# Kernel tuning notes

Measured on AMD Instinct MI355X. Metric: run time of the kernel, lower is better.

The kernel has to match this reference:

```python
import jax, jax.numpy as jnp
import numpy as np

D_MODEL = 512
N_HEADS = 8
HEAD_DIM = D_MODEL // N_HEADS
B, T = 128, 256


def setup_inputs() -> dict:
    key = jax.random.key(0)
    ks = jax.random.split(key, 5)
    s = 1.0 / np.sqrt(D_MODEL)
    return {
        "x": jax.random.normal(ks[0], (B, T, D_MODEL), dtype=jnp.float32),
        "W_qkv": jax.random.uniform(ks[1], (D_MODEL, 3 * D_MODEL), jnp.float32, -s, s),
        "b_qkv": jax.random.uniform(ks[2], (3 * D_MODEL,), jnp.float32, -s, s),
        "W_out": jax.random.uniform(ks[3], (D_MODEL, D_MODEL), jnp.float32, -s, s),
        "b_out": jax.random.uniform(ks[4], (D_MODEL,), jnp.float32, -s, s),
    }


def reference(x, W_qkv, b_qkv, W_out, b_out):
    Bsz, Tlen, C = x.shape
    H, hd = N_HEADS, HEAD_DIM
    qkv = x @ W_qkv + b_qkv                       # [B,T,3C]
    qkv = qkv.reshape(Bsz, Tlen, 3, H, hd).transpose(2, 0, 3, 1, 4)  # [3,B,H,T,hd]
    q, k, v = qkv[0], qkv[1], qkv[2]
    att = jnp.einsum('bhtd,bhsd->bhts', q, k) * (1.0 / np.sqrt(hd))  # [B,H,T,T]
    causal = jnp.tril(jnp.ones((Tlen, Tlen), dtype=bool))
    att = jnp.where(causal, att, -jnp.inf)
    att = jax.nn.softmax(att, axis=-1)
    y = jnp.einsum('bhts,bhsd->bhtd', att, v)     # [B,H,T,hd]
    y = y.transpose(0, 2, 1, 3).reshape(Bsz, Tlen, C)
    return y @ W_out + b_out
```

## Files before the change

kernel.cpp:

```cpp
#include <hip/hip_runtime.h>
#include <hip/hip_bf16.h>

typedef __attribute__((ext_vector_type(4))) float f32x4;
typedef __attribute__((ext_vector_type(8))) short s16x8;
typedef unsigned short u16;

__device__ __forceinline__ u16 f2bf(float f) {
    union { float f; unsigned int u; } a; a.f = f;
    unsigned int u = a.u;
    unsigned int lsb = (u >> 16) & 1u;
    u += 0x7fffu + lsb;
    return (u16)(u >> 16);
}

__device__ __forceinline__ void gll16(const u16* g, u16* l) {
    __builtin_amdgcn_global_load_lds(
        (const __attribute__((address_space(1))) unsigned int*)g,
        (__attribute__((address_space(3))) unsigned int*)l, 16, 0, 0);
}


__global__ __launch_bounds__(256) void cvt_all_kernel(const float* __restrict__ x,
                                                      const float* __restrict__ W_qkv,
                                                      const float* __restrict__ W_out,
                                                      u16* __restrict__ xb,
                                                      u16* __restrict__ WqkvT,
                                                      u16* __restrict__ WoutT) {
    int bid = blockIdx.x;
    if (bid < 16384) {
        int i = bid * 256 + threadIdx.x;
        float4 v = ((const float4*)x)[i];
        ushort4 o;
        o.x = f2bf(v.x); o.y = f2bf(v.y); o.z = f2bf(v.z); o.w = f2bf(v.w);
        ((ushort4*)xb)[i] = o;
    } else if (bid < 16768) {
        int id = (bid - 16384) * 256 + threadIdx.x;
        int n = id % 1536, kg = id / 1536;
        union { u16 h[8]; int4 v; } o;
#pragma unroll
        for (int e = 0; e < 8; ++e) o.h[e] = f2bf(W_qkv[(kg * 8 + e) * 1536 + n]);
        *(int4*)&WqkvT[n * 512 + kg * 8] = o.v;
    } else {
        int id = (bid - 16768) * 256 + threadIdx.x;
        int n = id % 512, kg = id / 512;
        union { u16 h[8]; int4 v; } o;
#pragma unroll
        for (int e = 0; e < 8; ++e) o.h[e] = f2bf(W_out[(kg * 8 + e) * 512 + n]);
        *(int4*)&WoutT[n * 512 + kg * 8] = o.v;
    }
}


template<int K>
__device__ __forceinline__ void stage256(const u16* __restrict__ A, const u16* __restrict__ Bt,
                                         int m0, int n0, int kt, u16* As, u16* Bs) {
    const int lane = threadIdx.x & 63, w = threadIdx.x >> 6;
    const int lr = lane >> 3, lg = lane & 7;
    const int sgA = lg ^ lr;
#pragma unroll
    for (int j = 0; j < 4; ++j) {
        const int blk = w * 4 + j;
        gll16(&A[(m0 + blk * 8 + lr) * K + kt + sgA * 8], &As[blk * 512]);
    }
#pragma unroll
    for (int j = 0; j < 4; ++j) {
        const int blk = w * 4 + j;
        const int sgB = lg ^ ((2 * j + (lr >> 2)) & 7);
        gll16(&Bt[(n0 + blk * 8 + lr) * K + kt + sgB * 8], &Bs[blk * 512]);
    }
}


template<int K>
__device__ __forceinline__ void gemm_tile256(const u16* __restrict__ A, const u16* __restrict__ Bt,
                                             int m0, int n0, u16* As, u16* Bs,
                                             f32x4 (&acc)[8][4]) {
    const int lane = threadIdx.x & 63, li = lane & 15, quad = lane >> 4;
    const int w = threadIdx.x >> 6;
    const int wr = w >> 2, wc = w & 3;
    const int sw = li & 7;

#pragma unroll
    for (int kt = 0; kt < K / 64; ++kt) {
        stage256<K>(A, Bt, m0, n0, kt * 64, As, Bs);
        __syncthreads();
#pragma unroll
        for (int kc = 0; kc < 2; ++kc) {
            s16x8 af[8], bf[4];
#pragma unroll
            for (int i = 0; i < 8; ++i)
                af[i] = *(const s16x8*)&As[(wr * 128 + i * 16 + li) * 64 + (((quad + kc * 4) ^ sw)) * 8];
#pragma unroll
            for (int j = 0; j < 4; ++j)
                bf[j] = *(const s16x8*)&Bs[(wc * 64 + li * 4 + j) * 64 + (((quad + kc * 4) ^ sw)) * 8];
#pragma unroll
            for (int i = 0; i < 8; ++i)
#pragma unroll
                for (int j = 0; j < 4; ++j)
                    acc[i][j] = __builtin_amdgcn_mfma_f32_16x16x32_bf16(af[i], bf[j], acc[i][j], 0, 0, 0);
        }
        __syncthreads();
    }
}


__global__ __launch_bounds__(512, 2) void gemm_qkv_kernel(const u16* __restrict__ xb,
                                                          const u16* __restrict__ WqkvT,
                                                          const float* __restrict__ b_qkv,
                                                          u16* __restrict__ Qb, u16* __restrict__ Kb,
                                                          u16* __restrict__ Vtb) {
    __shared__ __align__(16) u16 S[34816];
    u16* As = S;
    u16* Bs = S + 16384;

    f32x4 acc[8][4];
#pragma unroll
    for (int i = 0; i < 8; ++i)
#pragma unroll
        for (int j = 0; j < 4; ++j) acc[i][j] = {0.f, 0.f, 0.f, 0.f};

    const int id = blockIdx.x, xcd = id & 7, slot = id >> 3;
    const int mt = xcd * 16 + slot / 6, nt = slot % 6;
    const int m0 = mt * 256, n0 = nt * 256;
    gemm_tile256<512>(xb, WqkvT, m0, n0, As, Bs, acc);

    const int lane = threadIdx.x & 63, li = lane & 15, quad = lane >> 4;
    const int w = threadIdx.x >> 6, wr = w >> 2, wc = w & 3;
    const int c0 = n0 + wc * 64;
    float4 b4 = *(const float4*)&b_qkv[c0 + li * 4];

    if (n0 < 1024) {
        const int which = c0 >> 9, hh = (c0 >> 6) & 7;
        u16* __restrict__ dst = which ? Kb : Qb;
#pragma unroll
        for (int i = 0; i < 8; ++i)
#pragma unroll
            for (int r = 0; r < 4; ++r) {
                int row = m0 + wr * 128 + i * 16 + quad * 4 + r;
                int bb = row >> 8, tt = row & 255;
                int bh = (bb * 8 + hh) << 14;
                ushort4 o;
                o.x = f2bf(acc[i][0][r] + b4.x); o.y = f2bf(acc[i][1][r] + b4.y);
                o.z = f2bf(acc[i][2][r] + b4.z); o.w = f2bf(acc[i][3][r] + b4.w);
                *(ushort4*)&dst[bh + tt * 64 + li * 4] = o;
            }
    } else {
        const int hh = ((n0 >> 6) + wc) & 7;
        const size_t bh = ((size_t)(mt * 8 + hh)) << 14;
        u16* Rw = S + w * 4352;
#pragma unroll
        for (int h2 = 0; h2 < 2; ++h2) {
#pragma unroll
            for (int i = 0; i < 4; ++i)
#pragma unroll
                for (int r = 0; r < 4; ++r) {
                    int ai = h2 * 4 + i;
                    int rl = i * 16 + quad * 4 + r;
                    ushort4 o;
                    o.x = f2bf(acc[ai][0][r] + b4.x); o.y = f2bf(acc[ai][1][r] + b4.y);
                    o.z = f2bf(acc[ai][2][r] + b4.z); o.w = f2bf(acc[ai][3][r] + b4.w);
                    *(ushort4*)&Rw[rl * 68 + li * 4] = o;
                }
#pragma unroll
            for (int c = 0; c < 8; ++c) {
                int g = c * 64 + lane;
                int group = g >> 8;
                int d = (g & 255) >> 2;
                int sl8 = (g & 3) * 8;
                union { u16 h[8]; int4 v; } o;
#pragma unroll
                for (int e = 0; e < 8; ++e) o.h[e] = Rw[(group * 32 + sl8 + e) * 68 + d];
                *(int4*)&Vtb[bh + (wr * 4 + h2 * 2 + group) * 2048 + d * 32 + sl8] = o.v;
            }
        }
    }
}


__global__ __launch_bounds__(512, 2) void gemm_out_kernel(const u16* __restrict__ Yb,
                                                          const u16* __restrict__ WoutT,
                                                          const float* __restrict__ b_out,
                                                          float* __restrict__ out) {
    __shared__ __align__(16) u16 As[8192];
    __shared__ __align__(16) u16 Bs[16384];
    f32x4 acc[4][4];
#pragma unroll
    for (int i = 0; i < 4; ++i)
#pragma unroll
        for (int j = 0; j < 4; ++j) acc[i][j] = {0.f, 0.f, 0.f, 0.f};

    const int id = blockIdx.x, xcd = id & 7, slot = id >> 3;
    const int mt = xcd * 32 + (slot >> 1), nt = slot & 1;
    const int m0 = mt * 128, n0 = nt * 256;

    const int lane = threadIdx.x & 63, li = lane & 15, quad = lane >> 4;
    const int w = threadIdx.x >> 6, wr = w >> 2, wc = w & 3;
    const int sw = li & 7;
    const int lr = lane >> 3, lg = lane & 7;
    const int sgA = lg ^ lr;

#pragma unroll
    for (int kt = 0; kt < 8; ++kt) {
#pragma unroll
        for (int j = 0; j < 2; ++j) {
            const int blk = w * 2 + j;
            gll16(&Yb[(m0 + blk * 8 + lr) * 512 + kt * 64 + sgA * 8], &As[blk * 512]);
        }
#pragma unroll
        for (int j = 0; j < 4; ++j) {
            const int blk = w * 4 + j;
            const int sgB = lg ^ ((2 * j + (lr >> 2)) & 7);
            gll16(&WoutT[(n0 + blk * 8 + lr) * 512 + kt * 64 + sgB * 8], &Bs[blk * 512]);
        }
        __syncthreads();
#pragma unroll
        for (int kc = 0; kc < 2; ++kc) {
            s16x8 af[4], bf[4];
#pragma unroll
            for (int i = 0; i < 4; ++i)
                af[i] = *(const s16x8*)&As[(wr * 64 + i * 16 + li) * 64 + (((quad + kc * 4) ^ sw)) * 8];
#pragma unroll
            for (int j = 0; j < 4; ++j)
                bf[j] = *(const s16x8*)&Bs[(wc * 64 + li * 4 + j) * 64 + (((quad + kc * 4) ^ sw)) * 8];
#pragma unroll
            for (int i = 0; i < 4; ++i)
#pragma unroll
                for (int j = 0; j < 4; ++j)
                    acc[i][j] = __builtin_amdgcn_mfma_f32_16x16x32_bf16(af[i], bf[j], acc[i][j], 0, 0, 0);
        }
        __syncthreads();
    }

    const int c0 = n0 + wc * 64;
    float4 b4 = *(const float4*)&b_out[c0 + li * 4];
#pragma unroll
    for (int i = 0; i < 4; ++i)
#pragma unroll
        for (int r = 0; r < 4; ++r) {
            int row = m0 + wr * 64 + i * 16 + quad * 4 + r;
            float4 o;
            o.x = acc[i][0][r] + b4.x; o.y = acc[i][1][r] + b4.y;
            o.z = acc[i][2][r] + b4.z; o.w = acc[i][3][r] + b4.w;
            *(float4*)&out[row * 512 + c0 + li * 4] = o;
        }
}


__global__ __launch_bounds__(256, 2) void attn_kernel(const u16* __restrict__ Qb,
                                                      const u16* __restrict__ Kb,
                                                      const u16* __restrict__ Vtb,
                                                      u16* __restrict__ Yb) {
    __shared__ __align__(16) u16 Ks[256 * 64];
    __shared__ __align__(16) u16 pl[4 * 2 * 16 * 40];

    const int tid = threadIdx.x, wave = tid >> 6, lane = tid & 63, li = lane & 15, quad = lane >> 4;
    const int bhid = blockIdx.x;
    const int b = bhid >> 3, h = bhid & 7;
    const int bh = bhid << 14;

    s16x8 qf0 = *(const s16x8*)&Qb[bh + (wave * 16 + li) * 64 + quad * 8];
    s16x8 qf1 = *(const s16x8*)&Qb[bh + (wave * 16 + li) * 64 + 32 + quad * 8];

    {
        const int lr = lane >> 3;
        const int sg = (lane & 7) ^ lr;
#pragma unroll
        for (int j = 0; j < 8; ++j) {
            int blk = wave * 8 + j;
            gll16(&Kb[bh + (blk * 8 + lr) * 64 + sg * 8], &Ks[blk * 512]);
        }
    }
    __syncthreads();

    u16* plw = &pl[wave * 1280];

#pragma unroll
    for (int p = 0; p < 4; ++p) {
        const int qt = (p == 0) ? wave : (p == 1) ? (7 - wave) : (p == 2) ? (8 + wave) : (15 - wave);
        const int qrb = qt * 16;
        const int nst = qt + 1;

        f32x4 sacc[16];
#pragma unroll
        for (int st = 0; st < 16; ++st) sacc[st] = {0.f, 0.f, 0.f, 0.f};
        const int sw = li & 7;
#pragma unroll
        for (int g = 0; g < 4; ++g) {
            if (g * 4 < nst) {
                s16x8 kf[4][2];
#pragma unroll
                for (int t = 0; t < 4; ++t) {
                    if (g * 4 + t < nst) {
                        int rb = ((g * 4 + t) * 16 + li) * 64;
                        kf[t][0] = *(const s16x8*)&Ks[rb + ((quad    ) ^ sw) * 8];
                        kf[t][1] = *(const s16x8*)&Ks[rb + ((quad + 4) ^ sw) * 8];
                    }
                }
#pragma unroll
                for (int t = 0; t < 4; ++t) {
                    if (g * 4 + t < nst) {
                        sacc[g*4+t] = __builtin_amdgcn_mfma_f32_16x16x32_bf16(qf0, kf[t][0], sacc[g*4+t], 0, 0, 0);
                        sacc[g*4+t] = __builtin_amdgcn_mfma_f32_16x16x32_bf16(qf1, kf[t][1], sacc[g*4+t], 0, 0, 0);
                    }
                }
            }
        }

        s16x8 nqf0 = qf0, nqf1 = qf1;
        if (p < 3) {
            int nqt = (p == 0) ? (7 - wave) : (p == 1) ? (8 + wave) : (15 - wave);
            int nqrb = nqt * 16;
            nqf0 = *(const s16x8*)&Qb[bh + (nqrb + li) * 64 + quad * 8];
            nqf1 = *(const s16x8*)&Qb[bh + (nqrb + li) * 64 + 32 + quad * 8];
        }

        const int ns32 = (nst + 1) >> 1;
        float l[4] = {0.f, 0.f, 0.f, 0.f};
        f32x4 oacc[4];
#pragma unroll
        for (int dt = 0; dt < 4; ++dt) oacc[dt] = {0.f, 0.f, 0.f, 0.f};

        s16x8 vf[2][4];
#pragma unroll
        for (int dt = 0; dt < 4; ++dt)
            vf[0][dt] = *(const s16x8*)&Vtb[bh + (li * 4 + dt) * 32 + quad * 8];

#pragma unroll
        for (int c = 0; c < 8; ++c) {
            if (c < ns32) {
                if (c + 1 < ns32) {
#pragma unroll
                    for (int dt = 0; dt < 4; ++dt)
                        vf[(c + 1) & 1][dt] = *(const s16x8*)&Vtb[bh + (c + 1) * 2048 + (li * 4 + dt) * 32 + quad * 8];
                }
                u16* pb = plw + (c & 1) * 640;
#pragma unroll
                for (int half = 0; half < 2; ++half) {
                    int st = c * 2 + half;
                    int sg2 = st * 16 + li;
#pragma unroll
                    for (int r = 0; r < 4; ++r) {
                        int tg = qrb + quad * 4 + r;
                        float e = (st < nst && sg2 <= tg) ? __expf(sacc[st][r] * 0.125f) : 0.f;
                        l[r] += e;
                        pb[(quad * 4 + r) * 40 + half * 16 + li] = f2bf(e);
                    }
                }
                s16x8 pf = *(const s16x8*)&pb[li * 40 + quad * 8];
#pragma unroll
                for (int dt = 0; dt < 4; ++dt)
                    oacc[dt] = __builtin_amdgcn_mfma_f32_16x16x32_bf16(pf, vf[c & 1][dt], oacc[dt], 0, 0, 0);
            }
        }

#pragma unroll
        for (int d = 1; d < 16; d <<= 1)
#pragma unroll
            for (int r = 0; r < 4; ++r) l[r] += __shfl_xor(l[r], d, 64);

#pragma unroll
        for (int r = 0; r < 4; ++r) {
            int tg = qrb + quad * 4 + r;
            float inv = 1.0f / l[r];
            ushort4 o;
            o.x = f2bf(oacc[0][r] * inv); o.y = f2bf(oacc[1][r] * inv);
            o.z = f2bf(oacc[2][r] * inv); o.w = f2bf(oacc[3][r] * inv);
            *(ushort4*)&Yb[(b * 256 + tg) * 512 + h * 64 + li * 4] = o;
        }

        qf0 = nqf0; qf1 = nqf1;
    }
}


extern "C" void kernel_launch(void* const* d_in, const int* in_sizes, int n_in,
                              void* d_out, int out_size, void* d_ws, size_t ws_size,
                              hipStream_t stream) {
    const float* x     = (const float*)d_in[0];
    const float* W_qkv = (const float*)d_in[1];
    const float* b_qkv = (const float*)d_in[2];
    const float* W_out = (const float*)d_in[3];
    const float* b_out = (const float*)d_in[4];
    float* out = (float*)d_out;

    char* ws = (char*)d_ws;
    u16* Qb    = (u16*)(ws);
    u16* Kb    = (u16*)(ws + 33554432);
    u16* Vtb   = (u16*)(ws + 67108864);
    u16* WqkvT = (u16*)(ws + 100663296);
    u16* WoutT = (u16*)(ws + 102236160);
    u16* xb    = (u16*)(ws + 102760448);
    u16* Yb    = xb;
    if (ws_size < (size_t)136314880) return;

    cvt_all_kernel<<<16896, 256, 0, stream>>>(x, W_qkv, W_out, xb, WqkvT, WoutT);
    gemm_qkv_kernel<<<768, 512, 0, stream>>>(xb, WqkvT, b_qkv, Qb, Kb, Vtb);
    attn_kernel<<<1024, 256, 0, stream>>>(Qb, Kb, Vtb, Yb);
    gemm_out_kernel<<<512, 512, 0, stream>>>(Yb, WoutT, b_out, out);
}
```

Before: 264.5 us.

## Double-buffer LDS tiles in QKV GEMM and merge V-transpose epilogue

```diff
diff --git a/kernel.cpp b/kernel.cpp
--- a/kernel.cpp
+++ b/kernel.cpp
@@ -55,7 +55,8 @@
 __device__ __forceinline__ void stage256(const u16* __restrict__ A, const u16* __restrict__ Bt,
                                          int m0, int n0, int kt, u16* As, u16* Bs) {
     const int lane = threadIdx.x & 63, w = threadIdx.x >> 6;
-    const int lr = lane >> 3, lg = lane & 7;
+    const int lr = lane >> 3;
+    const int lg = lane & 7;
     const int sgA = lg ^ lr;
 #pragma unroll
     for (int j = 0; j < 4; ++j) {
@@ -70,29 +71,35 @@
     }
 }
 
-
 template<int K>
 __device__ __forceinline__ void gemm_tile256(const u16* __restrict__ A, const u16* __restrict__ Bt,
-                                             int m0, int n0, u16* As, u16* Bs,
+                                             int m0, int n0,
+                                             u16* As0, u16* Bs0, u16* As1, u16* Bs1,
                                              f32x4 (&acc)[8][4]) {
     const int lane = threadIdx.x & 63, li = lane & 15, quad = lane >> 4;
     const int w = threadIdx.x >> 6;
     const int wr = w >> 2, wc = w & 3;
     const int sw = li & 7;
 
+    stage256<K>(A, Bt, m0, n0, 0, As0, Bs0);
+    __syncthreads();
+
 #pragma unroll
     for (int kt = 0; kt < K / 64; ++kt) {
-        stage256<K>(A, Bt, m0, n0, kt * 64, As, Bs);
-        __syncthreads();
+        u16* Asc = (kt & 1) ? As1 : As0;
+        u16* Bsc = (kt & 1) ? Bs1 : Bs0;
+        if (kt + 1 < K / 64)
+            stage256<K>(A, Bt, m0, n0, (kt + 1) * 64,
+                        (kt & 1) ? As0 : As1, (kt & 1) ? Bs0 : Bs1);
 #pragma unroll
         for (int kc = 0; kc < 2; ++kc) {
             s16x8 af[8], bf[4];
 #pragma unroll
             for (int i = 0; i < 8; ++i)
-                af[i] = *(const s16x8*)&As[(wr * 128 + i * 16 + li) * 64 + (((quad + kc * 4) ^ sw)) * 8];
+                af[i] = *(const s16x8*)&Asc[(wr * 128 + i * 16 + li) * 64 + (((quad + kc * 4) ^ sw)) * 8];
 #pragma unroll
             for (int j = 0; j < 4; ++j)
-                bf[j] = *(const s16x8*)&Bs[(wc * 64 + li * 4 + j) * 64 + (((quad + kc * 4) ^ sw)) * 8];
+                bf[j] = *(const s16x8*)&Bsc[(wc * 64 + li * 4 + j) * 64 + (((quad + kc * 4) ^ sw)) * 8];
 #pragma unroll
             for (int i = 0; i < 8; ++i)
 #pragma unroll
@@ -109,9 +116,9 @@
                                                           const float* __restrict__ b_qkv,
                                                           u16* __restrict__ Qb, u16* __restrict__ Kb,
                                                           u16* __restrict__ Vtb) {
-    __shared__ __align__(16) u16 S[34816];
-    u16* As = S;
-    u16* Bs = S + 16384;
+    __shared__ __align__(16) u16 S[69632];
+    u16* As0 = S;          u16* Bs0 = S + 16384;
+    u16* As1 = S + 32768;  u16* Bs1 = S + 49152;
 
     f32x4 acc[8][4];
 #pragma unroll
@@ -122,7 +129,7 @@
     const int id = blockIdx.x, xcd = id & 7, slot = id >> 3;
     const int mt = xcd * 16 + slot / 6, nt = slot % 6;
     const int m0 = mt * 256, n0 = nt * 256;
-    gemm_tile256<512>(xb, WqkvT, m0, n0, As, Bs, acc);
+    gemm_tile256<512>(xb, WqkvT, m0, n0, As0, Bs0, As1, Bs1, acc);
 
     const int lane = threadIdx.x & 63, li = lane & 15, quad = lane >> 4;
     const int w = threadIdx.x >> 6, wr = w >> 2, wc = w & 3;
@@ -145,33 +152,30 @@
                 *(ushort4*)&dst[bh + tt * 64 + li * 4] = o;
             }
     } else {
+        u16* Rw = S + w * 8704;
+#pragma unroll
+        for (int i = 0; i < 8; ++i)
+#pragma unroll
+            for (int r = 0; r < 4; ++r) {
+                int rl = i * 16 + quad * 4 + r;
+                ushort4 o;
+                o.x = f2bf(acc[i][0][r] + b4.x); o.y = f2bf(acc[i][1][r] + b4.y);
+                o.z = f2bf(acc[i][2][r] + b4.z); o.w = f2bf(acc[i][3][r] + b4.w);
+                *(ushort4*)&Rw[rl * 68 + li * 4] = o;
+            }
+        __syncthreads();
         const int hh = ((n0 >> 6) + wc) & 7;
         const size_t bh = ((size_t)(mt * 8 + hh)) << 14;
-        u16* Rw = S + w * 4352;
-#pragma unroll
-        for (int h2 = 0; h2 < 2; ++h2) {
-#pragma unroll
-            for (int i = 0; i < 4; ++i)
-#pragma unroll
-                for (int r = 0; r < 4; ++r) {
-                    int ai = h2 * 4 + i;
-                    int rl = i * 16 + quad * 4 + r;
-                    ushort4 o;
-                    o.x = f2bf(acc[ai][0][r] + b4.x); o.y = f2bf(acc[ai][1][r] + b4.y);
-                    o.z = f2bf(acc[ai][2][r] + b4.z); o.w = f2bf(acc[ai][3][r] + b4.w);
-                    *(ushort4*)&Rw[rl * 68 + li * 4] = o;
-                }
-#pragma unroll
-            for (int c = 0; c < 8; ++c) {
-                int g = c * 64 + lane;
-                int group = g >> 8;
-                int d = (g & 255) >> 2;
-                int sl8 = (g & 3) * 8;
-                union { u16 h[8]; int4 v; } o;
-#pragma unroll
-                for (int e = 0; e < 8; ++e) o.h[e] = Rw[(group * 32 + sl8 + e) * 68 + d];
-                *(int4*)&Vtb[bh + (wr * 4 + h2 * 2 + group) * 2048 + d * 32 + sl8] = o.v;
-            }
+#pragma unroll
+        for (int c = 0; c < 16; ++c) {
+            int g = c * 64 + lane;
+            int group = g >> 8;
+            int d = (g & 255) >> 2;
+            int sl8 = (g & 3) * 8;
+            union { u16 h[8]; int4 v; } o;
+#pragma unroll
+            for (int e = 0; e < 8; ++e) o.h[e] = Rw[(group * 32 + sl8 + e) * 68 + d];
+            *(int4*)&Vtb[bh + (wr * 4 + group) * 2048 + d * 32 + sl8] = o.v;
         }
     }
 }
```

After: 256.1 us (median of 2 runs). -3.2%, faster.
